# Kernel optimization log

Hardware: AMD Instinct MI355X
Metric: run time of the kernel (lower is better)

## Reference

```python
import jax, jax.numpy as jnp
import numpy as np

N_AA = 20
A = 15
D_FEAT = 128
CA_IDX = 1
NUM_FUNCS = 3
FREQ_BANDS = jnp.array([1.0, 2.0, 3.0, 1.0, 0.5, 1.0 / 3.0], dtype=jnp.float32)


def setup_inputs() -> dict:
    key = jax.random.key(0)
    ks = jax.random.split(key, 16)
    b, L = 16, 1024
    d_in = D_FEAT + N_AA * A * 3 + 3 * (NUM_FUNCS * 2 * 2 + 1) + D_FEAT  # 1195
    inp = {
        "seq": jax.random.randint(ks[0], (b, L), 0, N_AA),
        "xyz": jax.random.normal(ks[1], (b, L, A, 3), dtype=jnp.float32),
        "dihedrals": jax.random.normal(ks[2], (b, L, 3), dtype=jnp.float32),
        "chain_idx": jax.random.randint(ks[3], (b, L), 0, 10),
        "orientation": jax.random.normal(ks[4], (b, L, 3, 3), dtype=jnp.float32),
        "atom_mask": jnp.ones((b, L, A), dtype=bool),
        "aa_emb": jax.random.normal(ks[5], (N_AA, D_FEAT), dtype=jnp.float32),
        "chain_emb": jax.random.normal(ks[6], (10, D_FEAT), dtype=jnp.float32).at[0].set(0.0),  # padding_idx=0
        "W1": jax.random.normal(ks[7], (d_in, 2 * D_FEAT), dtype=jnp.float32) * 0.02,
        "b1": jnp.zeros((2 * D_FEAT,), dtype=jnp.float32),
        "W2": jax.random.normal(ks[8], (2 * D_FEAT, D_FEAT), dtype=jnp.float32) * 0.02,
        "b2": jnp.zeros((D_FEAT,), dtype=jnp.float32),
        "W3": jax.random.normal(ks[9], (D_FEAT, D_FEAT), dtype=jnp.float32) * 0.02,
        "b3": jnp.zeros((D_FEAT,), dtype=jnp.float32),
        "W4": jax.random.normal(ks[10], (D_FEAT, D_FEAT), dtype=jnp.float32) * 0.02,
        "b4": jnp.zeros((D_FEAT,), dtype=jnp.float32),
    }
    return inp


def angular_encoding(x):
    # x: (..., d_in) -> (..., d_in * 13)
    xe = x[..., None]  # (..., d_in, 1)
    enc = jnp.concatenate([xe, jnp.sin(FREQ_BANDS * xe), jnp.cos(FREQ_BANDS * xe)], axis=-1)
    return enc.reshape(*x.shape[:-1], -1)


def reference(seq, xyz, dihedrals, chain_idx, orientation, atom_mask,
              aa_emb, chain_emb, W1, b1, W2, b2, W3, b3, W4, b4):
    b, L = seq.shape
    aa_type_feat = aa_emb[seq]  # (b, L, d_feat)

    # local coordinates relative to CA, rotated into local frame via O^T
    xyz_rel = xyz - xyz[:, :, CA_IDX:CA_IDX + 1, :]  # (b, L, A, 3)
    xyz_local = jnp.einsum('blji,blaj->blai', orientation, xyz_rel)  # O^T @ xyz_rel

    # one-hot select: place xyz_local in the slot of the residue's aa type
    onehot = jax.nn.one_hot(seq, N_AA, dtype=xyz.dtype)  # (b, L, 20)
    coord_feat = (onehot[:, :, :, None, None] * xyz_local[:, :, None, :, :]).reshape(b, L, N_AA * A * 3)

    dihedral_feat = angular_encoding(dihedrals)  # (b, L, 39)

    chain_feat = chain_emb[chain_idx] * (chain_idx != 0)[..., None].astype(xyz.dtype)  # padding_idx=0

    x = jnp.concatenate([aa_type_feat, coord_feat, dihedral_feat, chain_feat], axis=-1)
    h = jax.nn.relu(x @ W1 + b1)
    h = jax.nn.relu(h @ W2 + b2)
    h = jax.nn.relu(h @ W3 + b3)
    return h @ W4 + b4
```

## Files before the change

### kernel.cpp

```cpp
#include <hip/hip_runtime.h>
#include <math.h>

#define N_AA    20
#define NATOM   15
#define TM      32
#define MAXBL   16384
#define MAXBLK  (MAXBL / TM + N_AA)
#define NWAVE   16

#define FSX  104
#define HSX  264
#define H2SX 136

typedef __attribute__((ext_vector_type(8))) short bf16x8;
typedef __attribute__((ext_vector_type(4))) float f32x4;

#define W1F_SLOTS  (N_AA * 16 * 3 * 64)
#define W2F_SLOTS  (8 * 8 * 64)
#define W34F_SLOTS (8 * 4 * 64)
#define TOT_SLOTS  (W1F_SLOTS + W2F_SLOTS + 2 * W34F_SLOTS)

__device__ __forceinline__ unsigned short f2bf(float x) {
    unsigned u = __float_as_uint(x);
    return (unsigned short)((u + 0x7FFFu + ((u >> 16) & 1u)) >> 16);
}
__device__ __forceinline__ float bf2f(unsigned short h) {
    return __uint_as_float(((unsigned)h) << 16);
}
__device__ __forceinline__ void put2(unsigned short* H, unsigned short* L, int idx, float v) {
    unsigned short hi = f2bf(v);
    H[idx] = hi;
    L[idx] = f2bf(v - bf2f(hi));
}

__global__ __launch_bounds__(1024) void prep_kernel(
    const int* __restrict__ seq, const float* __restrict__ aa_emb,
    const float* __restrict__ chain_emb, const float* __restrict__ W1,
    const float* __restrict__ W2, const float* __restrict__ W3, const float* __restrict__ W4,
    int BL,
    float* __restrict__ aaT, float* __restrict__ chT,
    int* __restrict__ bucket_start, int* __restrict__ blk_type,
    int* __restrict__ blk_chunk, int* __restrict__ rowidx,
    unsigned short* __restrict__ W1fH, unsigned short* __restrict__ W1fL,
    unsigned short* __restrict__ W2fH, unsigned short* __restrict__ W2fL,
    unsigned short* __restrict__ W3fH, unsigned short* __restrict__ W3fL,
    unsigned short* __restrict__ W4fH, unsigned short* __restrict__ W4fL)
{
    const int t = threadIdx.x;
    const int b = blockIdx.x;

    if (b < 8) {
        const int tab = b * 4 + (t >> 8);
        const int col = t & 255;
        if (tab < 30) {
            if (tab < N_AA) {
                const float* e = aa_emb + tab * 128;
                float acc = 0.f;
                #pragma unroll 8
                for (int k = 0; k < 128; ++k)
                    acc += e[k] * W1[(size_t)k * 256 + col];
                aaT[tab * 256 + col] = acc;
            } else {
                const int c = tab - N_AA;
                const float* e = chain_emb + c * 128;
                float acc = 0.f;
                #pragma unroll 8
                for (int k = 0; k < 128; ++k)
                    acc += e[k] * W1[(size_t)(1067 + k) * 256 + col];
                chT[c * 256 + col] = acc;
            }
        }
        return;
    }

    if (b >= 9) {
        const int slot = (b - 9) * 1024 + t;
        if (slot >= TOT_SLOTS) return;
        float v[8];
        unsigned short *dH, *dL;
        if (slot < W1F_SLOTS) {
            const int g = slot / 3072, r1 = slot % 3072;
            const int tile = r1 / 192, chunk = (r1 / 64) % 3, lane = r1 % 64;
            const int n  = tile * 16 + (lane & 15);
            const int kb = chunk * 32 + (lane >> 4) * 8;
            #pragma unroll
            for (int j = 0; j < 8; ++j) {
                const int k = kb + j;
                float x = 0.f;
                if (k < 45)       x = W1[(size_t)(128 + g * 45 + k) * 256 + n];
                else if (k < 84)  x = W1[(size_t)(1028 + k - 45) * 256 + n];
                v[j] = x;
            }
            dH = W1fH + (size_t)slot * 8; dL = W1fL + (size_t)slot * 8;
        } else if (slot < W1F_SLOTS + W2F_SLOTS) {
            const int s = slot - W1F_SLOTS;
            const int tile = s / 512, chunk = (s / 64) % 8, lane = s % 64;
            const int n  = tile * 16 + (lane & 15);
            const int kb = chunk * 32 + (lane >> 4) * 8;
            #pragma unroll
            for (int j = 0; j < 8; ++j) v[j] = W2[(size_t)(kb + j) * 128 + n];
            dH = W2fH + (size_t)s * 8; dL = W2fL + (size_t)s * 8;
        } else if (slot < W1F_SLOTS + W2F_SLOTS + W34F_SLOTS) {
            const int s = slot - W1F_SLOTS - W2F_SLOTS;
            const int tile = s / 256, chunk = (s / 64) % 4, lane = s % 64;
            const int n  = tile * 16 + (lane & 15);
            const int kb = chunk * 32 + (lane >> 4) * 8;
            #pragma unroll
            for (int j = 0; j < 8; ++j) v[j] = W3[(size_t)(kb + j) * 128 + n];
            dH = W3fH + (size_t)s * 8; dL = W3fL + (size_t)s * 8;
        } else {
            const int s = slot - W1F_SLOTS - W2F_SLOTS - W34F_SLOTS;
            const int tile = s / 256, chunk = (s / 64) % 4, lane = s % 64;
            const int n  = tile * 16 + (lane & 15);
            const int kb = chunk * 32 + (lane >> 4) * 8;
            #pragma unroll
            for (int j = 0; j < 8; ++j) v[j] = W4[(size_t)(kb + j) * 128 + n];
            dH = W4fH + (size_t)s * 8; dL = W4fL + (size_t)s * 8;
        }
        #pragma unroll
        for (int j = 0; j < 8; ++j) {
            const unsigned short hi = f2bf(v[j]);
            dH[j] = hi;
            dL[j] = f2bf(v[j] - bf2f(hi));
        }
        return;
    }

    __shared__ int sseq[MAXBL];
    __shared__ int hist[NWAVE][N_AA];
    __shared__ int wcur[NWAVE][N_AA];
    __shared__ int bs[N_AA + 1];
    __shared__ int blkoff[N_AA + 1];

    const int w = t >> 6;
    for (int i = t; i < BL; i += 1024) sseq[i] = seq[i];
    if (t < NWAVE * N_AA) hist[t / N_AA][t % N_AA] = 0;
    __syncthreads();
    for (int i = t; i < BL; i += 1024) atomicAdd(&hist[w][sseq[i]], 1);
    __syncthreads();
    if (t == 0) {
        int runr = 0, runb = 0;
        for (int g = 0; g < N_AA; ++g) {
            int s = 0;
            #pragma unroll
            for (int ww = 0; ww < NWAVE; ++ww) s += hist[ww][g];
            bs[g] = runr; runr += s;
            blkoff[g] = runb; runb += (s + TM - 1) / TM;
        }
        bs[N_AA] = runr; blkoff[N_AA] = runb;
    }
    __syncthreads();
    if (t <= N_AA) bucket_start[t] = bs[t];
    if (t < NWAVE * N_AA) {
        const int w2 = t / N_AA, g2 = t % N_AA;
        int o = bs[g2];
        for (int ww = 0; ww < w2; ++ww) o += hist[ww][g2];
        wcur[w2][g2] = o;
    }
    const int nblk = blkoff[N_AA];
    for (int i = t; i < MAXBLK; i += 1024) {
        if (i < nblk) {
            int g = 0;
            while (blkoff[g + 1] <= i) ++g;
            blk_type[i]  = g;
            blk_chunk[i] = i - blkoff[g];
        } else blk_type[i] = -1;
    }
    __syncthreads();
    for (int i = t; i < BL; i += 1024) {
        const int pos = atomicAdd(&wcur[w][sseq[i]], 1);
        rowidx[pos] = i;
    }
}

__global__ __launch_bounds__(512, 4) void fused_kernel(
    const int* __restrict__ chain_idx, const float* __restrict__ xyz,
    const float* __restrict__ dihedrals, const float* __restrict__ orientation,
    const float* __restrict__ b1, const float* __restrict__ b2,
    const float* __restrict__ b3, const float* __restrict__ b4,
    const float* __restrict__ aaT, const float* __restrict__ chT,
    const int* __restrict__ bucket_start, const int* __restrict__ blk_type,
    const int* __restrict__ blk_chunk, const int* __restrict__ rowidx,
    const unsigned short* __restrict__ W1fH, const unsigned short* __restrict__ W1fL,
    const unsigned short* __restrict__ W2fH, const unsigned short* __restrict__ W2fL,
    const unsigned short* __restrict__ W3fH, const unsigned short* __restrict__ W3fL,
    const unsigned short* __restrict__ W4fH, const unsigned short* __restrict__ W4fL,
    float* __restrict__ out)
{
    __shared__ __align__(16) unsigned short smemA[2 * TM * HSX];
    __shared__ __align__(16) unsigned short smemB[2 * TM * H2SX];
    __shared__ int s_row[TM], s_rowld[TM], s_chain[TM];

    unsigned short* hAH   = smemA;
    unsigned short* hAL   = smemA + TM * HSX;
    unsigned short* featH = smemB;
    unsigned short* featL = smemB + TM * FSX;
    unsigned short* hBH   = smemB;
    unsigned short* hBL   = smemB + TM * H2SX;

    const int t = threadIdx.x;
    const int g = blk_type[blockIdx.x];
    if (g < 0) return;
    const int chunk  = blk_chunk[blockIdx.x];
    const int bstart = bucket_start[g] + chunk * TM;
    const int nrows  = min(TM, bucket_start[g + 1] - bstart);

    if (t < TM) {
        const bool valid = (t < nrows);
        const int rl = rowidx[valid ? (bstart + t) : bstart];
        s_row[t]   = valid ? rl : -1;
        s_rowld[t] = rl;
        s_chain[t] = chain_idx[rl];
    }
    __syncthreads();

    if (t < TM * NATOM) {
        const int r = t / NATOM, a = t % NATOM;
        const int rl = s_rowld[r];
        const float* xr = xyz + (size_t)rl * (NATOM * 3);
        const float cax = xr[3], cay = xr[4], caz = xr[5];
        const float rx = xr[a*3+0] - cax;
        const float ry = xr[a*3+1] - cay;
        const float rz = xr[a*3+2] - caz;
        const float* O = orientation + (size_t)rl * 9;
        put2(featH, featL, r * FSX + a*3 + 0, O[0]*rx + O[3]*ry + O[6]*rz);
        put2(featH, featL, r * FSX + a*3 + 1, O[1]*rx + O[4]*ry + O[7]*rz);
        put2(featH, featL, r * FSX + a*3 + 2, O[2]*rx + O[5]*ry + O[8]*rz);
    }
    if (t < TM * 3) {
        const int r = t / 3, d = t % 3;
        const float x = dihedrals[(size_t)s_rowld[r] * 3 + d];
        const int base = r * FSX + 45 + d * 13;
        const float F3 = (float)(1.0 / 3.0);
        const float s1 = sinf(x), c1 = cosf(x);
        put2(featH, featL, base + 0, x);
        put2(featH, featL, base + 1, s1);           put2(featH, featL, base + 2, sinf(2.f*x));
        put2(featH, featL, base + 3, sinf(3.f*x));  put2(featH, featL, base + 4, s1);
        put2(featH, featL, base + 5, sinf(0.5f*x)); put2(featH, featL, base + 6, sinf(F3*x));
        put2(featH, featL, base + 7, c1);           put2(featH, featL, base + 8, cosf(2.f*x));
        put2(featH, featL, base + 9, cosf(3.f*x));  put2(featH, featL, base +10, c1);
        put2(featH, featL, base +11, cosf(0.5f*x)); put2(featH, featL, base +12, cosf(F3*x));
    }
    if (t < TM) {
        #pragma unroll
        for (int k = 84; k < 96; ++k) { featH[t * FSX + k] = 0; featL[t * FSX + k] = 0; }
    }
    __syncthreads();

    const int wave = t >> 6, lane = t & 63, quad = lane >> 4, nid = lane & 15;
    const f32x4 zero = {0.f, 0.f, 0.f, 0.f};

    {
        f32x4 acc[2][2] = {{zero, zero}, {zero, zero}};
        for (int c = 0; c < 3; ++c) {
            const bf16x8 aH0 = *(const bf16x8*)(featH + nid * FSX + c * 32 + quad * 8);
            const bf16x8 aL0 = *(const bf16x8*)(featL + nid * FSX + c * 32 + quad * 8);
            const bf16x8 aH1 = *(const bf16x8*)(featH + (16 + nid) * FSX + c * 32 + quad * 8);
            const bf16x8 aL1 = *(const bf16x8*)(featL + (16 + nid) * FSX + c * 32 + quad * 8);
            #pragma unroll
            for (int tt = 0; tt < 2; ++tt) {
                const size_t off = ((size_t)((g * 16 + (wave * 2 + tt)) * 3 + c) * 64 + lane) * 8;
                const bf16x8 bH = *(const bf16x8*)(W1fH + off);
                const bf16x8 bL = *(const bf16x8*)(W1fL + off);
                acc[0][tt] = __builtin_amdgcn_mfma_f32_16x16x32_bf16(aH0, bH, acc[0][tt], 0, 0, 0);
                acc[0][tt] = __builtin_amdgcn_mfma_f32_16x16x32_bf16(aH0, bL, acc[0][tt], 0, 0, 0);
                acc[0][tt] = __builtin_amdgcn_mfma_f32_16x16x32_bf16(aL0, bH, acc[0][tt], 0, 0, 0);
                acc[1][tt] = __builtin_amdgcn_mfma_f32_16x16x32_bf16(aH1, bH, acc[1][tt], 0, 0, 0);
                acc[1][tt] = __builtin_amdgcn_mfma_f32_16x16x32_bf16(aH1, bL, acc[1][tt], 0, 0, 0);
                acc[1][tt] = __builtin_amdgcn_mfma_f32_16x16x32_bf16(aL1, bH, acc[1][tt], 0, 0, 0);
            }
        }
        #pragma unroll
        for (int tt = 0; tt < 2; ++tt) {
            const int j = (wave * 2 + tt) * 16 + nid;
            const float cb = b1[j] + aaT[g * 256 + j];
            #pragma unroll
            for (int rt = 0; rt < 2; ++rt) {
                #pragma unroll
                for (int r = 0; r < 4; ++r) {
                    const int row = rt * 16 + quad * 4 + r;
                    float v = acc[rt][tt][r] + cb + chT[s_chain[row] * 256 + j];
                    v = fmaxf(v, 0.f);
                    put2(hAH, hAL, row * HSX + j, v);
                }
            }
        }
    }
    __syncthreads();

    {
        f32x4 acc[2] = {zero, zero};
        for (int c = 0; c < 8; ++c) {
            const bf16x8 aH0 = *(const bf16x8*)(hAH + nid * HSX + c * 32 + quad * 8);
            const bf16x8 aL0 = *(const bf16x8*)(hAL + nid * HSX + c * 32 + quad * 8);
            const bf16x8 aH1 = *(const bf16x8*)(hAH + (16 + nid) * HSX + c * 32 + quad * 8);
            const bf16x8 aL1 = *(const bf16x8*)(hAL + (16 + nid) * HSX + c * 32 + quad * 8);
            const size_t off = ((size_t)(wave * 8 + c) * 64 + lane) * 8;
            const bf16x8 bH = *(const bf16x8*)(W2fH + off);
            const bf16x8 bL = *(const bf16x8*)(W2fL + off);
            acc[0] = __builtin_amdgcn_mfma_f32_16x16x32_bf16(aH0, bH, acc[0], 0, 0, 0);
            acc[0] = __builtin_amdgcn_mfma_f32_16x16x32_bf16(aH0, bL, acc[0], 0, 0, 0);
            acc[0] = __builtin_amdgcn_mfma_f32_16x16x32_bf16(aL0, bH, acc[0], 0, 0, 0);
            acc[1] = __builtin_amdgcn_mfma_f32_16x16x32_bf16(aH1, bH, acc[1], 0, 0, 0);
            acc[1] = __builtin_amdgcn_mfma_f32_16x16x32_bf16(aH1, bL, acc[1], 0, 0, 0);
            acc[1] = __builtin_amdgcn_mfma_f32_16x16x32_bf16(aL1, bH, acc[1], 0, 0, 0);
        }
        __syncthreads();
        const int j = wave * 16 + nid;
        const float bb = b2[j];
        #pragma unroll
        for (int rt = 0; rt < 2; ++rt) {
            #pragma unroll
            for (int r = 0; r < 4; ++r) {
                const int row = rt * 16 + quad * 4 + r;
                float v = fmaxf(acc[rt][r] + bb, 0.f);
                put2(hBH, hBL, row * H2SX + j, v);
            }
        }
    }
    __syncthreads();

    {
        f32x4 acc[2] = {zero, zero};
        for (int c = 0; c < 4; ++c) {
            const bf16x8 aH0 = *(const bf16x8*)(hBH + nid * H2SX + c * 32 + quad * 8);
            const bf16x8 aL0 = *(const bf16x8*)(hBL + nid * H2SX + c * 32 + quad * 8);
            const bf16x8 aH1 = *(const bf16x8*)(hBH + (16 + nid) * H2SX + c * 32 + quad * 8);
            const bf16x8 aL1 = *(const bf16x8*)(hBL + (16 + nid) * H2SX + c * 32 + quad * 8);
            const size_t off = ((size_t)(wave * 4 + c) * 64 + lane) * 8;
            const bf16x8 bH = *(const bf16x8*)(W3fH + off);
            const bf16x8 bL = *(const bf16x8*)(W3fL + off);
            acc[0] = __builtin_amdgcn_mfma_f32_16x16x32_bf16(aH0, bH, acc[0], 0, 0, 0);
            acc[0] = __builtin_amdgcn_mfma_f32_16x16x32_bf16(aH0, bL, acc[0], 0, 0, 0);
            acc[0] = __builtin_amdgcn_mfma_f32_16x16x32_bf16(aL0, bH, acc[0], 0, 0, 0);
            acc[1] = __builtin_amdgcn_mfma_f32_16x16x32_bf16(aH1, bH, acc[1], 0, 0, 0);
            acc[1] = __builtin_amdgcn_mfma_f32_16x16x32_bf16(aH1, bL, acc[1], 0, 0, 0);
            acc[1] = __builtin_amdgcn_mfma_f32_16x16x32_bf16(aL1, bH, acc[1], 0, 0, 0);
        }
        const int j = wave * 16 + nid;
        const float bb = b3[j];
        #pragma unroll
        for (int rt = 0; rt < 2; ++rt) {
            #pragma unroll
            for (int r = 0; r < 4; ++r) {
                const int row = rt * 16 + quad * 4 + r;
                float v = fmaxf(acc[rt][r] + bb, 0.f);
                put2(hAH, hAL, row * HSX + j, v);
            }
        }
    }
    __syncthreads();

    {
        f32x4 acc[2] = {zero, zero};
        for (int c = 0; c < 4; ++c) {
            const bf16x8 aH0 = *(const bf16x8*)(hAH + nid * HSX + c * 32 + quad * 8);
            const bf16x8 aL0 = *(const bf16x8*)(hAL + nid * HSX + c * 32 + quad * 8);
            const bf16x8 aH1 = *(const bf16x8*)(hAH + (16 + nid) * HSX + c * 32 + quad * 8);
            const bf16x8 aL1 = *(const bf16x8*)(hAL + (16 + nid) * HSX + c * 32 + quad * 8);
            const size_t off = ((size_t)(wave * 4 + c) * 64 + lane) * 8;
            const bf16x8 bH = *(const bf16x8*)(W4fH + off);
            const bf16x8 bL = *(const bf16x8*)(W4fL + off);
            acc[0] = __builtin_amdgcn_mfma_f32_16x16x32_bf16(aH0, bH, acc[0], 0, 0, 0);
            acc[0] = __builtin_amdgcn_mfma_f32_16x16x32_bf16(aH0, bL, acc[0], 0, 0, 0);
            acc[0] = __builtin_amdgcn_mfma_f32_16x16x32_bf16(aL0, bH, acc[0], 0, 0, 0);
            acc[1] = __builtin_amdgcn_mfma_f32_16x16x32_bf16(aH1, bH, acc[1], 0, 0, 0);
            acc[1] = __builtin_amdgcn_mfma_f32_16x16x32_bf16(aH1, bL, acc[1], 0, 0, 0);
            acc[1] = __builtin_amdgcn_mfma_f32_16x16x32_bf16(aL1, bH, acc[1], 0, 0, 0);
        }
        const int j = wave * 16 + nid;
        const float bb = b4[j];
        #pragma unroll
        for (int rt = 0; rt < 2; ++rt) {
            #pragma unroll
            for (int r = 0; r < 4; ++r) {
                const int row = rt * 16 + quad * 4 + r;
                const int orow = s_row[row];
                if (orow >= 0) out[(size_t)orow * 128 + j] = acc[rt][r] + bb;
            }
        }
    }
}

extern "C" void kernel_launch(void* const* d_in, const int* in_sizes, int n_in,
                              void* d_out, int out_size, void* d_ws, size_t ws_size,
                              hipStream_t stream) {
    const int*   seq    = (const int*)d_in[0];
    const float* xyz    = (const float*)d_in[1];
    const float* dihed  = (const float*)d_in[2];
    const int*   chain  = (const int*)d_in[3];
    const float* orient = (const float*)d_in[4];
    const float* aa_emb = (const float*)d_in[6];
    const float* ch_emb = (const float*)d_in[7];
    const float* W1 = (const float*)d_in[8];
    const float* b1 = (const float*)d_in[9];
    const float* W2 = (const float*)d_in[10];
    const float* b2 = (const float*)d_in[11];
    const float* W3 = (const float*)d_in[12];
    const float* b3 = (const float*)d_in[13];
    const float* W4 = (const float*)d_in[14];
    const float* b4 = (const float*)d_in[15];
    float* out = (float*)d_out;

    const int BL = in_sizes[0];

    char* p = (char*)d_ws;
    float* aaT = (float*)p;            p += 20 * 256 * 4;
    float* chT = (float*)p;            p += 10 * 256 * 4;
    int* bucket_start = (int*)p;       p += 32 * 4;
    int* blk_type     = (int*)p;       p += MAXBLK * 4;
    int* blk_chunk    = (int*)p;       p += MAXBLK * 4;
    int* rowidx       = (int*)p;       p += MAXBL * 4;
    p += ((16 - ((uintptr_t)p & 15)) & 15);
    unsigned short* W1fH = (unsigned short*)p; p += (size_t)W1F_SLOTS * 8 * 2;
    unsigned short* W1fL = (unsigned short*)p; p += (size_t)W1F_SLOTS * 8 * 2;
    unsigned short* W2fH = (unsigned short*)p; p += (size_t)W2F_SLOTS * 8 * 2;
    unsigned short* W2fL = (unsigned short*)p; p += (size_t)W2F_SLOTS * 8 * 2;
    unsigned short* W3fH = (unsigned short*)p; p += (size_t)W34F_SLOTS * 8 * 2;
    unsigned short* W3fL = (unsigned short*)p; p += (size_t)W34F_SLOTS * 8 * 2;
    unsigned short* W4fH = (unsigned short*)p; p += (size_t)W34F_SLOTS * 8 * 2;
    unsigned short* W4fL = (unsigned short*)p;

    const int nprep  = 9 + (TOT_SLOTS + 1023) / 1024;
    const int nfused = BL / TM + N_AA;

    prep_kernel<<<nprep, 1024, 0, stream>>>(seq, aa_emb, ch_emb, W1, W2, W3, W4, BL,
                                            aaT, chT, bucket_start, blk_type, blk_chunk, rowidx,
                                            W1fH, W1fL, W2fH, W2fL, W3fH, W3fL, W4fH, W4fL);
    fused_kernel<<<nfused, 512, 0, stream>>>(chain, xyz, dihed, orient,
                                             b1, b2, b3, b4, aaT, chT,
                                             bucket_start, blk_type, blk_chunk, rowidx,
                                             W1fH, W1fL, W2fH, W2fL, W3fH, W3fL, W4fH, W4fL,
                                             out);
}
```

Measured before the change: 124.2 us.

## Halve block size, double per-wave tiles, prefetch weights, remap blocks across XCDs

The fused MLP kernel now launches 256 threads per block instead of 512, and each wave computes twice as many output column tiles per layer. The first weight chunk of each layer is loaded into registers ahead of time, overlapping with feature construction or the previous layer's epilogue. Block indices are also remapped so that consecutive logical blocks, which share the same amino-acid weight bucket, land on the same XCD for better L2 reuse. The cost is higher register pressure and less parallelism per block.

```diff
diff --git a/kernel.cpp b/kernel.cpp
--- a/kernel.cpp
+++ b/kernel.cpp
@@ -173,7 +173,7 @@
     }
 }
 
-__global__ __launch_bounds__(512, 4) void fused_kernel(
+__global__ __launch_bounds__(256, 3) void fused_kernel(
     const int* __restrict__ chain_idx, const float* __restrict__ xyz,
     const float* __restrict__ dihedrals, const float* __restrict__ orientation,
     const float* __restrict__ b1, const float* __restrict__ b2,
@@ -199,11 +199,27 @@
     unsigned short* hBL   = smemB + TM * H2SX;
 
     const int t = threadIdx.x;
-    const int g = blk_type[blockIdx.x];
+
+    const int nwg = gridDim.x;
+    const int q = nwg >> 3, r = nwg & 7;
+    const int xcd = blockIdx.x & 7, loc = blockIdx.x >> 3;
+    const int bid = (xcd < r ? xcd * (q + 1) : r * (q + 1) + (xcd - r) * q) + loc;
+
+    const int g = blk_type[bid];
     if (g < 0) return;
-    const int chunk  = blk_chunk[blockIdx.x];
+    const int chunk  = blk_chunk[bid];
     const int bstart = bucket_start[g] + chunk * TM;
     const int nrows  = min(TM, bucket_start[g + 1] - bstart);
+
+    const int wave = t >> 6, lane = t & 63, quad = lane >> 4, nid = lane & 15;
+
+    bf16x8 p1H[4], p1L[4];
+    #pragma unroll
+    for (int tt = 0; tt < 4; ++tt) {
+        const size_t off = ((size_t)((g * 16 + (wave * 4 + tt)) * 3 + 0) * 64 + lane) * 8;
+        p1H[tt] = *(const bf16x8*)(W1fH + off);
+        p1L[tt] = *(const bf16x8*)(W1fL + off);
+    }
 
     if (t < TM) {
         const bool valid = (t < nrows);
@@ -214,23 +230,23 @@
     }
     __syncthreads();
 
-    if (t < TM * NATOM) {
-        const int r = t / NATOM, a = t % NATOM;
-        const int rl = s_rowld[r];
+    for (int i = t; i < TM * NATOM; i += 256) {
+        const int rr = i / NATOM, a = i % NATOM;
+        const int rl = s_rowld[rr];
         const float* xr = xyz + (size_t)rl * (NATOM * 3);
         const float cax = xr[3], cay = xr[4], caz = xr[5];
         const float rx = xr[a*3+0] - cax;
         const float ry = xr[a*3+1] - cay;
         const float rz = xr[a*3+2] - caz;
         const float* O = orientation + (size_t)rl * 9;
-        put2(featH, featL, r * FSX + a*3 + 0, O[0]*rx + O[3]*ry + O[6]*rz);
-        put2(featH, featL, r * FSX + a*3 + 1, O[1]*rx + O[4]*ry + O[7]*rz);
-        put2(featH, featL, r * FSX + a*3 + 2, O[2]*rx + O[5]*ry + O[8]*rz);
+        put2(featH, featL, rr * FSX + a*3 + 0, O[0]*rx + O[3]*ry + O[6]*rz);
+        put2(featH, featL, rr * FSX + a*3 + 1, O[1]*rx + O[4]*ry + O[7]*rz);
+        put2(featH, featL, rr * FSX + a*3 + 2, O[2]*rx + O[5]*ry + O[8]*rz);
     }
     if (t < TM * 3) {
-        const int r = t / 3, d = t % 3;
-        const float x = dihedrals[(size_t)s_rowld[r] * 3 + d];
-        const int base = r * FSX + 45 + d * 13;
+        const int rr = t / 3, d = t % 3;
+        const float x = dihedrals[(size_t)s_rowld[rr] * 3 + d];
+        const int base = rr * FSX + 45 + d * 13;
         const float F3 = (float)(1.0 / 3.0);
         const float s1 = sinf(x), c1 = cosf(x);
         put2(featH, featL, base + 0, x);
@@ -247,21 +263,26 @@
     }
     __syncthreads();
 
-    const int wave = t >> 6, lane = t & 63, quad = lane >> 4, nid = lane & 15;
     const f32x4 zero = {0.f, 0.f, 0.f, 0.f};
 
+    bf16x8 p2H[2], p2L[2];
     {
-        f32x4 acc[2][2] = {{zero, zero}, {zero, zero}};
+        f32x4 acc[2][4] = {{zero, zero, zero, zero}, {zero, zero, zero, zero}};
+        #pragma unroll
         for (int c = 0; c < 3; ++c) {
             const bf16x8 aH0 = *(const bf16x8*)(featH + nid * FSX + c * 32 + quad * 8);
             const bf16x8 aL0 = *(const bf16x8*)(featL + nid * FSX + c * 32 + quad * 8);
             const bf16x8 aH1 = *(const bf16x8*)(featH + (16 + nid) * FSX + c * 32 + quad * 8);
             const bf16x8 aL1 = *(const bf16x8*)(featL + (16 + nid) * FSX + c * 32 + quad * 8);
             #pragma unroll
-            for (int tt = 0; tt < 2; ++tt) {
-                const size_t off = ((size_t)((g * 16 + (wave * 2 + tt)) * 3 + c) * 64 + lane) * 8;
-                const bf16x8 bH = *(const bf16x8*)(W1fH + off);
-                const bf16x8 bL = *(const bf16x8*)(W1fL + off);
+            for (int tt = 0; tt < 4; ++tt) {
+                bf16x8 bH, bL;
+                if (c == 0) { bH = p1H[tt]; bL = p1L[tt]; }
+                else {
+                    const size_t off = ((size_t)((g * 16 + (wave * 4 + tt)) * 3 + c) * 64 + lane) * 8;
+                    bH = *(const bf16x8*)(W1fH + off);
+                    bL = *(const bf16x8*)(W1fL + off);
+                }
                 acc[0][tt] = __builtin_amdgcn_mfma_f32_16x16x32_bf16(aH0, bH, acc[0][tt], 0, 0, 0);
                 acc[0][tt] = __builtin_amdgcn_mfma_f32_16x16x32_bf16(aH0, bL, acc[0][tt], 0, 0, 0);
                 acc[0][tt] = __builtin_amdgcn_mfma_f32_16x16x32_bf16(aL0, bH, acc[0][tt], 0, 0, 0);
@@ -272,14 +293,20 @@
         }
         #pragma unroll
         for (int tt = 0; tt < 2; ++tt) {
-            const int j = (wave * 2 + tt) * 16 + nid;
+            const size_t off = ((size_t)((wave * 2 + tt) * 8 + 0) * 64 + lane) * 8;
+            p2H[tt] = *(const bf16x8*)(W2fH + off);
+            p2L[tt] = *(const bf16x8*)(W2fL + off);
+        }
+        #pragma unroll
+        for (int tt = 0; tt < 4; ++tt) {
+            const int j = (wave * 4 + tt) * 16 + nid;
             const float cb = b1[j] + aaT[g * 256 + j];
             #pragma unroll
             for (int rt = 0; rt < 2; ++rt) {
                 #pragma unroll
-                for (int r = 0; r < 4; ++r) {
-                    const int row = rt * 16 + quad * 4 + r;
-                    float v = acc[rt][tt][r] + cb + chT[s_chain[row] * 256 + j];
+                for (int rr = 0; rr < 4; ++rr) {
+                    const int row = rt * 16 + quad * 4 + rr;
+                    float v = acc[rt][tt][rr] + cb + chT[s_chain[row] * 256 + j];
                     v = fmaxf(v, 0.f);
                     put2(hAH, hAL, row * HSX + j, v);
                 }
@@ -288,95 +315,141 @@
     }
     __syncthreads();
 
+    bf16x8 p3H[2], p3L[2];
     {
-        f32x4 acc[2] = {zero, zero};
+        f32x4 acc[2][2] = {{zero, zero}, {zero, zero}};
+        #pragma unroll
         for (int c = 0; c < 8; ++c) {
             const bf16x8 aH0 = *(const bf16x8*)(hAH + nid * HSX + c * 32 + quad * 8);
             const bf16x8 aL0 = *(const bf16x8*)(hAL + nid * HSX + c * 32 + quad * 8);
             const bf16x8 aH1 = *(const bf16x8*)(hAH + (16 + nid) * HSX + c * 32 + quad * 8);
             const bf16x8 aL1 = *(const bf16x8*)(hAL + (16 + nid) * HSX + c * 32 + quad * 8);
-            const size_t off = ((size_t)(wave * 8 + c) * 64 + lane) * 8;
-            const bf16x8 bH = *(const bf16x8*)(W2fH + off);
-            const bf16x8 bL = *(const bf16x8*)(W2fL + off);
-            acc[0] = __builtin_amdgcn_mfma_f32_16x16x32_bf16(aH0, bH, acc[0], 0, 0, 0);
-            acc[0] = __builtin_amdgcn_mfma_f32_16x16x32_bf16(aH0, bL, acc[0], 0, 0, 0);
-            acc[0] = __builtin_amdgcn_mfma_f32_16x16x32_bf16(aL0, bH, acc[0], 0, 0, 0);
-            acc[1] = __builtin_amdgcn_mfma_f32_16x16x32_bf16(aH1, bH, acc[1], 0, 0, 0);
-            acc[1] = __builtin_amdgcn_mfma_f32_16x16x32_bf16(aH1, bL, acc[1], 0, 0, 0);
-            acc[1] = __builtin_amdgcn_mfma_f32_16x16x32_bf16(aL1, bH, acc[1], 0, 0, 0);
-        }
-        __syncthreads();
-        const int j = wave * 16 + nid;
-        const float bb = b2[j];
-        #pragma unroll
-        for (int rt = 0; rt < 2; ++rt) {
-            #pragma unroll
-            for (int r = 0; r < 4; ++r) {
-                const int row = rt * 16 + quad * 4 + r;
-                float v = fmaxf(acc[rt][r] + bb, 0.f);
-                put2(hBH, hBL, row * H2SX + j, v);
-            }
-        }
-    }
-    __syncthreads();
-
+            #pragma unroll
+            for (int tt = 0; tt < 2; ++tt) {
+                bf16x8 bH, bL;
+                if (c == 0) { bH = p2H[tt]; bL = p2L[tt]; }
+                else {
+                    const size_t off = ((size_t)((wave * 2 + tt) * 8 + c) * 64 + lane) * 8;
+                    bH = *(const bf16x8*)(W2fH + off);
+                    bL = *(const bf16x8*)(W2fL + off);
+                }
+                acc[0][tt] = __builtin_amdgcn_mfma_f32_16x16x32_bf16(aH0, bH, acc[0][tt], 0, 0, 0);
+                acc[0][tt] = __builtin_amdgcn_mfma_f32_16x16x32_bf16(aH0, bL, acc[0][tt], 0, 0, 0);
+                acc[0][tt] = __builtin_amdgcn_mfma_f32_16x16x32_bf16(aL0, bH, acc[0][tt], 0, 0, 0);
+                acc[1][tt] = __builtin_amdgcn_mfma_f32_16x16x32_bf16(aH1, bH, acc[1][tt], 0, 0, 0);
+                acc[1][tt] = __builtin_amdgcn_mfma_f32_16x16x32_bf16(aH1, bL, acc[1][tt], 0, 0, 0);
+                acc[1][tt] = __builtin_amdgcn_mfma_f32_16x16x32_bf16(aL1, bH, acc[1][tt], 0, 0, 0);
+            }
+        }
+        #pragma unroll
+        for (int tt = 0; tt < 2; ++tt) {
+            const size_t off = ((size_t)((wave * 2 + tt) * 4 + 0) * 64 + lane) * 8;
+            p3H[tt] = *(const bf16x8*)(W3fH + off);
+            p3L[tt] = *(const bf16x8*)(W3fL + off);
+        }
+        #pragma unroll
+        for (int tt = 0; tt < 2; ++tt) {
+            const int j = (wave * 2 + tt) * 16 + nid;
+            const float bb = b2[j];
+            #pragma unroll
+            for (int rt = 0; rt < 2; ++rt) {
+                #pragma unroll
+                for (int rr = 0; rr < 4; ++rr) {
+                    const int row = rt * 16 + quad * 4 + rr;
+                    float v = fmaxf(acc[rt][tt][rr] + bb, 0.f);
+                    put2(hBH, hBL, row * H2SX + j, v);
+                }
+            }
+        }
+    }
+    __syncthreads();
+
+    bf16x8 p4H[2], p4L[2];
     {
-        f32x4 acc[2] = {zero, zero};
+        f32x4 acc[2][2] = {{zero, zero}, {zero, zero}};
+        #pragma unroll
         for (int c = 0; c < 4; ++c) {
             const bf16x8 aH0 = *(const bf16x8*)(hBH + nid * H2SX + c * 32 + quad * 8);
             const bf16x8 aL0 = *(const bf16x8*)(hBL + nid * H2SX + c * 32 + quad * 8);
             const bf16x8 aH1 = *(const bf16x8*)(hBH + (16 + nid) * H2SX + c * 32 + quad * 8);
             const bf16x8 aL1 = *(const bf16x8*)(hBL + (16 + nid) * H2SX + c * 32 + quad * 8);
-            const size_t off = ((size_t)(wave * 4 + c) * 64 + lane) * 8;
-            const bf16x8 bH = *(const bf16x8*)(W3fH + off);
-            const bf16x8 bL = *(const bf16x8*)(W3fL + off);
-            acc[0] = __builtin_amdgcn_mfma_f32_16x16x32_bf16(aH0, bH, acc[0], 0, 0, 0);
-            acc[0] = __builtin_amdgcn_mfma_f32_16x16x32_bf16(aH0, bL, acc[0], 0, 0, 0);
-            acc[0] = __builtin_amdgcn_mfma_f32_16x16x32_bf16(aL0, bH, acc[0], 0, 0, 0);
-            acc[1] = __builtin_amdgcn_mfma_f32_16x16x32_bf16(aH1, bH, acc[1], 0, 0, 0);
-            acc[1] = __builtin_amdgcn_mfma_f32_16x16x32_bf16(aH1, bL, acc[1], 0, 0, 0);
-            acc[1] = __builtin_amdgcn_mfma_f32_16x16x32_bf16(aL1, bH, acc[1], 0, 0, 0);
-        }
-        const int j = wave * 16 + nid;
-        const float bb = b3[j];
-        #pragma unroll
-        for (int rt = 0; rt < 2; ++rt) {
-            #pragma unroll
-            for (int r = 0; r < 4; ++r) {
-                const int row = rt * 16 + quad * 4 + r;
-                float v = fmaxf(acc[rt][r] + bb, 0.f);
-                put2(hAH, hAL, row * HSX + j, v);
+            #pragma unroll
+            for (int tt = 0; tt < 2; ++tt) {
+                bf16x8 bH, bL;
+                if (c == 0) { bH = p3H[tt]; bL = p3L[tt]; }
+                else {
+                    const size_t off = ((size_t)((wave * 2 + tt) * 4 + c) * 64 + lane) * 8;
+                    bH = *(const bf16x8*)(W3fH + off);
+                    bL = *(const bf16x8*)(W3fL + off);
+                }
+                acc[0][tt] = __builtin_amdgcn_mfma_f32_16x16x32_bf16(aH0, bH, acc[0][tt], 0, 0, 0);
+                acc[0][tt] = __builtin_amdgcn_mfma_f32_16x16x32_bf16(aH0, bL, acc[0][tt], 0, 0, 0);
+                acc[0][tt] = __builtin_amdgcn_mfma_f32_16x16x32_bf16(aL0, bH, acc[0][tt], 0, 0, 0);
+                acc[1][tt] = __builtin_amdgcn_mfma_f32_16x16x32_bf16(aH1, bH, acc[1][tt], 0, 0, 0);
+                acc[1][tt] = __builtin_amdgcn_mfma_f32_16x16x32_bf16(aH1, bL, acc[1][tt], 0, 0, 0);
+                acc[1][tt] = __builtin_amdgcn_mfma_f32_16x16x32_bf16(aL1, bH, acc[1][tt], 0, 0, 0);
+            }
+        }
+        #pragma unroll
+        for (int tt = 0; tt < 2; ++tt) {
+            const size_t off = ((size_t)((wave * 2 + tt) * 4 + 0) * 64 + lane) * 8;
+            p4H[tt] = *(const bf16x8*)(W4fH + off);
+            p4L[tt] = *(const bf16x8*)(W4fL + off);
+        }
+        #pragma unroll
+        for (int tt = 0; tt < 2; ++tt) {
+            const int j = (wave * 2 + tt) * 16 + nid;
+            const float bb = b3[j];
+            #pragma unroll
+            for (int rt = 0; rt < 2; ++rt) {
+                #pragma unroll
+                for (int rr = 0; rr < 4; ++rr) {
+                    const int row = rt * 16 + quad * 4 + rr;
+                    float v = fmaxf(acc[rt][tt][rr] + bb, 0.f);
+                    put2(hAH, hAL, row * HSX + j, v);
+                }
             }
         }
     }
     __syncthreads();
 
     {
-        f32x4 acc[2] = {zero, zero};
+        f32x4 acc[2][2] = {{zero, zero}, {zero, zero}};
+        #pragma unroll
         for (int c = 0; c < 4; ++c) {
             const bf16x8 aH0 = *(const bf16x8*)(hAH + nid * HSX + c * 32 + quad * 8);
             const bf16x8 aL0 = *(const bf16x8*)(hAL + nid * HSX + c * 32 + quad * 8);
             const bf16x8 aH1 = *(const bf16x8*)(hAH + (16 + nid) * HSX + c * 32 + quad * 8);
             const bf16x8 aL1 = *(const bf16x8*)(hAL + (16 + nid) * HSX + c * 32 + quad * 8);
-            const size_t off = ((size_t)(wave * 4 + c) * 64 + lane) * 8;
-            const bf16x8 bH = *(const bf16x8*)(W4fH + off);
-            const bf16x8 bL = *(const bf16x8*)(W4fL + off);
-            acc[0] = __builtin_amdgcn_mfma_f32_16x16x32_bf16(aH0, bH, acc[0], 0, 0, 0);
-            acc[0] = __builtin_amdgcn_mfma_f32_16x16x32_bf16(aH0, bL, acc[0], 0, 0, 0);
-            acc[0] = __builtin_amdgcn_mfma_f32_16x16x32_bf16(aL0, bH, acc[0], 0, 0, 0);
-            acc[1] = __builtin_amdgcn_mfma_f32_16x16x32_bf16(aH1, bH, acc[1], 0, 0, 0);
-            acc[1] = __builtin_amdgcn_mfma_f32_16x16x32_bf16(aH1, bL, acc[1], 0, 0, 0);
-            acc[1] = __builtin_amdgcn_mfma_f32_16x16x32_bf16(aL1, bH, acc[1], 0, 0, 0);
-        }
-        const int j = wave * 16 + nid;
-        const float bb = b4[j];
-        #pragma unroll
-        for (int rt = 0; rt < 2; ++rt) {
-            #pragma unroll
-            for (int r = 0; r < 4; ++r) {
-                const int row = rt * 16 + quad * 4 + r;
-                const int orow = s_row[row];
-                if (orow >= 0) out[(size_t)orow * 128 + j] = acc[rt][r] + bb;
+            #pragma unroll
+            for (int tt = 0; tt < 2; ++tt) {
+                bf16x8 bH, bL;
+                if (c == 0) { bH = p4H[tt]; bL = p4L[tt]; }
+                else {
+                    const size_t off = ((size_t)((wave * 2 + tt) * 4 + c) * 64 + lane) * 8;
+                    bH = *(const bf16x8*)(W4fH + off);
+                    bL = *(const bf16x8*)(W4fL + off);
+                }
+                acc[0][tt] = __builtin_amdgcn_mfma_f32_16x16x32_bf16(aH0, bH, acc[0][tt], 0, 0, 0);
+                acc[0][tt] = __builtin_amdgcn_mfma_f32_16x16x32_bf16(aH0, bL, acc[0][tt], 0, 0, 0);
+                acc[0][tt] = __builtin_amdgcn_mfma_f32_16x16x32_bf16(aL0, bH, acc[0][tt], 0, 0, 0);
+                acc[1][tt] = __builtin_amdgcn_mfma_f32_16x16x32_bf16(aH1, bH, acc[1][tt], 0, 0, 0);
+                acc[1][tt] = __builtin_amdgcn_mfma_f32_16x16x32_bf16(aH1, bL, acc[1][tt], 0, 0, 0);
+                acc[1][tt] = __builtin_amdgcn_mfma_f32_16x16x32_bf16(aL1, bH, acc[1][tt], 0, 0, 0);
+            }
+        }
+        #pragma unroll
+        for (int tt = 0; tt < 2; ++tt) {
+            const int j = (wave * 2 + tt) * 16 + nid;
+            const float bb = b4[j];
+            #pragma unroll
+            for (int rt = 0; rt < 2; ++rt) {
+                #pragma unroll
+                for (int rr = 0; rr < 4; ++rr) {
+                    const int row = rt * 16 + quad * 4 + rr;
+                    const int orow = s_row[row];
+                    if (orow >= 0) out[(size_t)orow * 128 + j] = acc[rt][tt][rr] + bb;
+                }
             }
         }
     }
@@ -427,7 +500,7 @@
     prep_kernel<<<nprep, 1024, 0, stream>>>(seq, aa_emb, ch_emb, W1, W2, W3, W4, BL,
                                             aaT, chT, bucket_start, blk_type, blk_chunk, rowidx,
                                             W1fH, W1fL, W2fH, W2fL, W3fH, W3fL, W4fH, W4fL);
-    fused_kernel<<<nfused, 512, 0, stream>>>(chain, xyz, dihed, orient,
+    fused_kernel<<<nfused, 256, 0, stream>>>(chain, xyz, dihed, orient,
                                              b1, b2, b3, b4, aaT, chT,
                                              bucket_start, blk_type, blk_chunk, rowidx,
                                              W1fH, W1fL, W2fH, W2fL, W3fH, W3fL, W4fH, W4fL,
```

After: 121.6 us. 1.02x faster.
